# Kernel optimization log

Hardware: AMD Instinct MI355X
Metric: run time of the kernel (lower is better)

Reference implementation:

```python
import jax, jax.numpy as jnp
import numpy as np

N = 100000      # nodes (cells)
E = 1600000     # edges (kNN graph, avg degree 16)
DIM_IN = 128    # input features per cell
H = 8           # heads
C1 = 8          # per-head channels, layer 1 (concat -> 64)
DIM_OUT = 10    # classes (concat=False -> mean over heads)
NEG_SLOPE = 0.2


def setup_inputs() -> dict:
    key = jax.random.key(0)
    ks = jax.random.split(key, 10)
    s = 0.1
    return {
        "x": jax.random.normal(ks[0], (N, DIM_IN), dtype=jnp.float32),
        "edge_index": jax.random.randint(ks[1], (2, E), 0, N, dtype=jnp.int64),
        "W1": jax.random.normal(ks[2], (DIM_IN, H * C1), dtype=jnp.float32) * s,
        "a_src1": jax.random.normal(ks[3], (H, C1), dtype=jnp.float32) * s,
        "a_dst1": jax.random.normal(ks[4], (H, C1), dtype=jnp.float32) * s,
        "b1": jnp.zeros((H * C1,), dtype=jnp.float32),
        "W2": jax.random.normal(ks[5], (H * C1, H * DIM_OUT), dtype=jnp.float32) * s,
        "a_src2": jax.random.normal(ks[6], (H, DIM_OUT), dtype=jnp.float32) * s,
        "a_dst2": jax.random.normal(ks[7], (H, DIM_OUT), dtype=jnp.float32) * s,
        "b2": jnp.zeros((DIM_OUT,), dtype=jnp.float32),
    }


def _gat_layer(x, src, dst, W, a_src, a_dst, bias, concat, n):
    """PyG-style GATConv: gather -> edge attention -> segment softmax -> scatter."""
    h_, c_ = a_src.shape
    h = (x @ W).reshape(n, h_, c_)                       # [N, H, C]
    alpha_s = jnp.einsum('nhc,hc->nh', h, a_src)         # [N, H]
    alpha_d = jnp.einsum('nhc,hc->nh', h, a_dst)         # [N, H]
    # per-edge logits; PyG: message from src j to dst i, softmax over dst
    e = jax.nn.leaky_relu(alpha_s[src] + alpha_d[dst], NEG_SLOPE)  # [E, H]
    e_max = jax.ops.segment_max(e, dst, num_segments=n)            # [N, H]
    e = jnp.exp(e - e_max[dst])
    denom = jax.ops.segment_sum(e, dst, num_segments=n)            # [N, H]
    alpha = e / denom[dst]                                          # [E, H]
    msg = h[src] * alpha[:, :, None]                                # [E, H, C]
    out = jax.ops.segment_sum(msg, dst, num_segments=n)             # [N, H, C]
    out = out.reshape(n, h_ * c_) if concat else out.mean(axis=1)
    return out + bias


def reference(x, edge_index, W1, a_src1, a_dst1, b1, W2, a_src2, a_dst2, b2):
    n = x.shape[0]
    loops = jnp.arange(n, dtype=edge_index.dtype)
    src = jnp.concatenate([edge_index[0], loops])  # PyG adds self-loops by default
    dst = jnp.concatenate([edge_index[1], loops])
    h = _gat_layer(x, src, dst, W1, a_src1, a_dst1, b1, True, n)   # [N, 64]
    h = jax.nn.elu(h)
    h = _gat_layer(h, src, dst, W2, a_src2, a_dst2, b2, False, n)  # [N, dim_out]
    return jax.nn.log_softmax(h, axis=1)
```

## Files before the change

### kernel.cpp

```cpp
#include <hip/hip_runtime.h>
#include <hip/hip_bf16.h>
#include <cstdint>

#define CAP 64
#define SLICES 8
#define CHUNK_EDGES 8192

__device__ __forceinline__ float lrelu(float v) { return fmaxf(v, 0.2f * v); }

typedef float f32x2 __attribute__((ext_vector_type(2)));
__device__ __forceinline__ float2 q2f(unsigned short u) {
    f32x2 v = __builtin_amdgcn_cvt_pk_f32_fp8((int)u, false);
    return make_float2(v.x, v.y);
}
__device__ __forceinline__ int f2q4(float a, float b, float c, float d) {
    int p = __builtin_amdgcn_cvt_pk_fp8_f32(a, b, 0, false);
    p = __builtin_amdgcn_cvt_pk_fp8_f32(c, d, p, true);
    return p;
}
__device__ __forceinline__ float b2f(unsigned short u) { return __uint_as_float(((unsigned)u) << 16); }
__device__ __forceinline__ unsigned short f2b(float f) {
    unsigned u = __float_as_uint(f);
    return (unsigned short)((u + 0x7FFFu + ((u >> 16) & 1u)) >> 16);
}

__global__ __launch_bounds__(256, 8) void k_bg(const int* __restrict__ ei, int E, int N,
                                               int* __restrict__ cnt, int* __restrict__ bucket,
                                               const float* __restrict__ x,
                                               const float* __restrict__ W,
                                               const float* __restrict__ asrc,
                                               const float* __restrict__ adst,
                                               unsigned char* __restrict__ h1q,
                                               float* __restrict__ als, float* __restrict__ ald,
                                               int buildBlocks) {
    __shared__ float xs[32 * 132];
    if ((int)blockIdx.x < buildBlocks) {
        const int s = blockIdx.x & (SLICES - 1);
        const int chunk = blockIdx.x >> 3;
        const int sliceN = (N + SLICES - 1) / SLICES;
        const int lo = s * sliceN;
        const int hi = min(N, lo + sliceN);
        const int base = chunk * CHUNK_EDGES;
        const int end = min(base + CHUNK_EDGES, E);
        for (int e0 = base + (int)threadIdx.x * 4; e0 < end; e0 += 1024) {
            if (e0 + 4 <= end) {
                int4 d = *(const int4*)(ei + E + e0);
                int4 sv = *(const int4*)(ei + e0);
                if (d.x >= lo && d.x < hi) { int a = atomicAdd(&cnt[d.x], 1); if (a < CAP) bucket[(size_t)d.x * CAP + a] = sv.x; }
                if (d.y >= lo && d.y < hi) { int a = atomicAdd(&cnt[d.y], 1); if (a < CAP) bucket[(size_t)d.y * CAP + a] = sv.y; }
                if (d.z >= lo && d.z < hi) { int a = atomicAdd(&cnt[d.z], 1); if (a < CAP) bucket[(size_t)d.z * CAP + a] = sv.z; }
                if (d.w >= lo && d.w < hi) { int a = atomicAdd(&cnt[d.w], 1); if (a < CAP) bucket[(size_t)d.w * CAP + a] = sv.w; }
            } else {
                for (int e = e0; e < end; ++e) {
                    int d = ei[E + e];
                    if (d >= lo && d < hi) {
                        int a = atomicAdd(&cnt[d], 1);
                        if (a < CAP) bucket[(size_t)d * CAP + a] = ei[e];
                    }
                }
            }
        }
        return;
    }
    const int t = threadIdx.x;
    const int rowBase = ((int)blockIdx.x - buildBlocks) * 32;
#pragma unroll
    for (int i = 0; i < 4; ++i) {
        int g = i * 256 + t;
        int r = g >> 5, c4 = (g & 31) << 2;
        float4 v = make_float4(0.f, 0.f, 0.f, 0.f);
        int row = rowBase + r;
        if (row < N) v = *(const float4*)(x + (size_t)row * 128 + c4);
        *(float4*)(&xs[r * 132 + c4]) = v;
    }
    __syncthreads();
    const int tx = t & 15;
    const int ty = t >> 4;
    float acc[2][4] = {};
#pragma unroll 2
    for (int kc = 0; kc < 32; ++kc) {
        float4 a[2];
#pragma unroll
        for (int i = 0; i < 2; ++i) a[i] = *(const float4*)(&xs[(2 * ty + i) * 132 + kc * 4]);
        float4 w[4];
#pragma unroll
        for (int kk = 0; kk < 4; ++kk) w[kk] = *(const float4*)(W + (size_t)(kc * 4 + kk) * 64 + tx * 4);
#pragma unroll
        for (int i = 0; i < 2; ++i) {
            const float* ai = (const float*)&a[i];
#pragma unroll
            for (int j = 0; j < 4; ++j) {
                acc[i][j] += ai[0] * ((const float*)&w[0])[j]
                           + ai[1] * ((const float*)&w[1])[j]
                           + ai[2] * ((const float*)&w[2])[j]
                           + ai[3] * ((const float*)&w[3])[j];
            }
        }
    }
    const int h = tx >> 1;
    float4 av = *(const float4*)(asrc + tx * 4);
    float4 dv = *(const float4*)(adst + tx * 4);
#pragma unroll
    for (int i = 0; i < 2; ++i) {
        int row = rowBase + 2 * ty + i;
        float ps = acc[i][0] * av.x + acc[i][1] * av.y + acc[i][2] * av.z + acc[i][3] * av.w;
        float pd = acc[i][0] * dv.x + acc[i][1] * dv.y + acc[i][2] * dv.z + acc[i][3] * dv.w;
        ps += __shfl_xor(ps, 1);
        pd += __shfl_xor(pd, 1);
        if (row < N) {
            *(int*)(h1q + (size_t)row * 64 + tx * 4) = f2q4(acc[i][0], acc[i][1], acc[i][2], acc[i][3]);
            if ((tx & 1) == 0) {
                als[(size_t)row * 8 + h] = ps;
                ald[(size_t)row * 8 + h] = pd;
            }
        }
    }
}

__global__ __launch_bounds__(256) void k_gemm2(const float* __restrict__ hin,
                                               const float* __restrict__ W,
                                               const float* __restrict__ asrc,
                                               const float* __restrict__ adst,
                                               unsigned char* __restrict__ h2q,
                                               float* __restrict__ ald, int N) {
    __shared__ float xs[64 * 68];
    __shared__ float wt[80 * 68];
    const int t = threadIdx.x;
    const int rowBase = blockIdx.x * 64;
#pragma unroll
    for (int i = 0; i < 4; ++i) {
        int g = i * 256 + t;
        int r = g >> 4, c4 = (g & 15) << 2;
        float4 v = make_float4(0.f, 0.f, 0.f, 0.f);
        int row = rowBase + r;
        if (row < N) v = *(const float4*)(hin + (size_t)row * 64 + c4);
        *(float4*)(&xs[r * 68 + c4]) = v;
    }
#pragma unroll
    for (int i = 0; i < 20; ++i) {
        int g = i * 256 + t;
        int k = g / 80, c = g % 80;
        wt[c * 68 + k] = W[g];
    }
    __syncthreads();
    const int tx = t & 15;
    const int ty = t >> 4;
    float acc[4][5] = {};
#pragma unroll 4
    for (int kc = 0; kc < 16; ++kc) {
        float4 a[4];
#pragma unroll
        for (int i = 0; i < 4; ++i) a[i] = *(const float4*)(&xs[(4 * ty + i) * 68 + kc * 4]);
        float4 w[5];
#pragma unroll
        for (int j = 0; j < 5; ++j) w[j] = *(const float4*)(&wt[(5 * tx + j) * 68 + kc * 4]);
#pragma unroll
        for (int i = 0; i < 4; ++i) {
#pragma unroll
            for (int j = 0; j < 5; ++j) {
                acc[i][j] += a[i].x * w[j].x + a[i].y * w[j].y + a[i].z * w[j].z + a[i].w * w[j].w;
            }
        }
    }
    const int h = tx >> 1;
    float a2[5], d2[5];
#pragma unroll
    for (int j = 0; j < 5; ++j) { a2[j] = asrc[tx * 5 + j]; d2[j] = adst[tx * 5 + j]; }
    __syncthreads();
    unsigned char* qs = (unsigned char*)xs;
#pragma unroll
    for (int i = 0; i < 4; ++i) {
        int row = rowBase + 4 * ty + i;
        float ps = 0.f, pd = 0.f;
#pragma unroll
        for (int j = 0; j < 5; ++j) { ps += acc[i][j] * a2[j]; pd += acc[i][j] * d2[j]; }
        ps += __shfl_xor(ps, 1);
        pd += __shfl_xor(pd, 1);
        int p0 = __builtin_amdgcn_cvt_pk_fp8_f32(acc[i][0], acc[i][1], 0, false);
        int p1 = __builtin_amdgcn_cvt_pk_fp8_f32(acc[i][2], acc[i][3], 0, false);
        int p2 = __builtin_amdgcn_cvt_pk_fp8_f32(acc[i][4], acc[i][4], 0, false);
        unsigned char* q = qs + (4 * ty + i) * 96 + h * 12 + (tx & 1) * 5;
        q[0] = (unsigned char)(p0 & 0xFF);
        q[1] = (unsigned char)((p0 >> 8) & 0xFF);
        q[2] = (unsigned char)(p1 & 0xFF);
        q[3] = (unsigned char)((p1 >> 8) & 0xFF);
        q[4] = (unsigned char)(p2 & 0xFF);
        if ((tx & 1) == 0) {
            *(unsigned short*)(qs + (size_t)(4 * ty + i) * 96 + h * 12 + 10) = f2b(ps);
            if (row < N) ald[(size_t)row * 8 + h] = pd;
        }
    }
    __syncthreads();
    for (int g = t; g < 1536; g += 256) {
        int row = g / 24;
        if (rowBase + row < N)
            *(unsigned int*)(h2q + (size_t)rowBase * 96 + (size_t)g * 4) = ((unsigned int*)qs)[g];
    }
}

__global__ __launch_bounds__(256) void k_agg1(const int* __restrict__ cnt, const int* __restrict__ bucket,
                                              const unsigned char* __restrict__ h1q,
                                              const float* __restrict__ als, const float* __restrict__ ald,
                                              const float* __restrict__ b1,
                                              float* __restrict__ helu, int N) {
    int w = threadIdx.x >> 6, lane = threadIdx.x & 63;
    int e = lane >> 3, h = lane & 7;
    int n = blockIdx.x * 4 + w;
    bool act = n < N;
    float acc[8] = {};
    float den = 0.f;
    if (act) {
        float aldh = ald[(size_t)n * 8 + h];
        auto proc = [&](int s) {
            const unsigned char* row = h1q + (size_t)s * 64 + h * 8;
            int m0 = *(const int*)(row);
            int m1 = *(const int*)(row + 4);
            float a_s = als[(size_t)s * 8 + h];
            float wl = __expf(lrelu(a_s + aldh));
            den += wl;
            f32x2 v;
            v = __builtin_amdgcn_cvt_pk_f32_fp8(m0, false); acc[0] += wl * v.x; acc[1] += wl * v.y;
            v = __builtin_amdgcn_cvt_pk_f32_fp8(m0, true);  acc[2] += wl * v.x; acc[3] += wl * v.y;
            v = __builtin_amdgcn_cvt_pk_f32_fp8(m1, false); acc[4] += wl * v.x; acc[5] += wl * v.y;
            v = __builtin_amdgcn_cvt_pk_f32_fp8(m1, true);  acc[6] += wl * v.x; acc[7] += wl * v.y;
        };
        if (e == 0) proc(n);
        int k = min(cnt[n], CAP);
        const int* bp = bucket + (size_t)n * CAP;
        int i = e;
        int s = (i < k) ? bp[i] : -1;
        while (i < k) {
            int inext = i + 8;
            int snext = (inext < k) ? bp[inext] : -1;
            proc(s);
            i = inext; s = snext;
        }
    }
#pragma unroll
    for (int off = 8; off < 64; off <<= 1) {
        den += __shfl_xor(den, off);
#pragma unroll
        for (int j = 0; j < 8; ++j) acc[j] += __shfl_xor(acc[j], off);
    }
    if (act && e == 0) {
        float inv = 1.f / den;
        float o[8];
#pragma unroll
        for (int j = 0; j < 8; ++j) {
            float v = acc[j] * inv + b1[h * 8 + j];
            o[j] = v > 0.f ? v : __expf(v) - 1.f;
        }
        *(float4*)(helu + (size_t)n * 64 + h * 8)     = make_float4(o[0], o[1], o[2], o[3]);
        *(float4*)(helu + (size_t)n * 64 + h * 8 + 4) = make_float4(o[4], o[5], o[6], o[7]);
    }
}

__global__ __launch_bounds__(256) void k_agg2(const int* __restrict__ cnt, const int* __restrict__ bucket,
                                              const unsigned char* __restrict__ h2q,
                                              const float* __restrict__ ald,
                                              const float* __restrict__ b2,
                                              float* __restrict__ out, int N) {
    __shared__ float sm[4][80];
    int w = threadIdx.x >> 6, lane = threadIdx.x & 63;
    int e = lane >> 3, h = lane & 7;
    int n = blockIdx.x * 4 + w;
    bool act = n < N;
    float acc[10] = {};
    float den = 0.f;
    if (act) {
        float aldh = ald[(size_t)n * 8 + h];
        auto proc = [&](const unsigned char* row) {
            int m0 = *(const int*)(row);
            int m1 = *(const int*)(row + 4);
            int m2 = *(const int*)(row + 8);
            float a_s = b2f((unsigned short)(((unsigned)m2) >> 16));
            float wl = __expf(lrelu(a_s + aldh));
            den += wl;
            f32x2 v;
            v = __builtin_amdgcn_cvt_pk_f32_fp8(m0, false); acc[0] += wl * v.x; acc[1] += wl * v.y;
            v = __builtin_amdgcn_cvt_pk_f32_fp8(m0, true);  acc[2] += wl * v.x; acc[3] += wl * v.y;
            v = __builtin_amdgcn_cvt_pk_f32_fp8(m1, false); acc[4] += wl * v.x; acc[5] += wl * v.y;
            v = __builtin_amdgcn_cvt_pk_f32_fp8(m1, true);  acc[6] += wl * v.x; acc[7] += wl * v.y;
            v = __builtin_amdgcn_cvt_pk_f32_fp8(m2, false); acc[8] += wl * v.x; acc[9] += wl * v.y;
        };
        if (e == 0) proc(h2q + (size_t)n * 96 + h * 12);
        int k = min(cnt[n], CAP);
        const int* bp = bucket + (size_t)n * CAP;
        int i = e;
        int s = (i < k) ? bp[i] : -1;
        while (i < k) {
            int inext = i + 8;
            int snext = (inext < k) ? bp[inext] : -1;
            proc(h2q + (size_t)s * 96 + h * 12);
            i = inext; s = snext;
        }
    }
#pragma unroll
    for (int off = 8; off < 64; off <<= 1) {
        den += __shfl_xor(den, off);
#pragma unroll
        for (int j = 0; j < 10; ++j) acc[j] += __shfl_xor(acc[j], off);
    }
    if (act && e == 0) {
        float inv = 1.f / den;
#pragma unroll
        for (int j = 0; j < 10; ++j) sm[w][h * 10 + j] = acc[j] * inv;
    }
    __syncthreads();
    float m = 0.f;
    if (act && lane < 10) {
#pragma unroll
        for (int hh = 0; hh < 8; ++hh) m += sm[w][hh * 10 + lane];
        m = m * 0.125f + b2[lane];
    }
    __syncthreads();
    if (act && lane < 10) sm[w][lane] = m;
    __syncthreads();
    if (act && lane < 10) {
        float mx = -1e30f;
#pragma unroll
        for (int c = 0; c < 10; ++c) mx = fmaxf(mx, sm[w][c]);
        float ssum = 0.f;
#pragma unroll
        for (int c = 0; c < 10; ++c) ssum += __expf(sm[w][c] - mx);
        out[(size_t)n * 10 + lane] = m - mx - __logf(ssum);
    }
}

extern "C" void kernel_launch(void* const* d_in, const int* in_sizes, int n_in,
                              void* d_out, int out_size, void* d_ws, size_t ws_size,
                              hipStream_t stream) {
    const float* x     = (const float*)d_in[0];
    const int*   ei    = (const int*)d_in[1];
    const float* W1    = (const float*)d_in[2];
    const float* asrc1 = (const float*)d_in[3];
    const float* adst1 = (const float*)d_in[4];
    const float* b1    = (const float*)d_in[5];
    const float* W2    = (const float*)d_in[6];
    const float* asrc2 = (const float*)d_in[7];
    const float* adst2 = (const float*)d_in[8];
    const float* b2    = (const float*)d_in[9];
    float* out = (float*)d_out;

    int N = in_sizes[0] / 128;
    int E = in_sizes[1] / 2;

    char* base = (char*)d_ws;
    size_t off = 0;
    auto alloc = [&](size_t bytes) {
        char* p = base + off;
        off = (off + bytes + 255) & ~(size_t)255;
        return p;
    };
    int*            cnt    = (int*)alloc((size_t)N * 4);
    int*            bucket = (int*)alloc((size_t)N * CAP * 4);
    float*          helu   = (float*)alloc((size_t)N * 64 * 4);
    unsigned char*  hq     = (unsigned char*)alloc((size_t)N * 96);
    float*          als    = (float*)alloc((size_t)N * 8 * 4);
    float*          ald    = (float*)alloc((size_t)N * 8 * 4);
    (void)ws_size; (void)n_in; (void)out_size;

    (void)hipMemsetAsync(cnt, 0, (size_t)N * 4, stream);
    int chunks = (E + CHUNK_EDGES - 1) / CHUNK_EDGES;
    int buildBlocks = chunks * SLICES;
    int gemmBlocks = (N + 31) / 32;
    k_bg<<<buildBlocks + gemmBlocks, 256, 0, stream>>>(ei, E, N, cnt, bucket,
                                                       x, W1, asrc1, adst1, hq, als, ald, buildBlocks);
    k_agg1<<<(N + 3) / 4, 256, 0, stream>>>(cnt, bucket, hq, als, ald, b1, helu, N);
    k_gemm2<<<(N + 63) / 64, 256, 0, stream>>>(helu, W2, asrc2, adst2, hq, ald, N);
    k_agg2<<<(N + 3) / 4, 256, 0, stream>>>(cnt, bucket, hq, ald, b2, out, N);
}
```

Before: 356.9 us.

## Split fused build/GEMM kernel, shrink edge chunks, store source logits as bf16

Splits the combined bucket-build and layer-1 GEMM kernel into two separate launches. The build kernel now uses smaller edge chunks, giving more blocks and more parallelism for the atomic bucket fill. Source attention logits are stored as bf16 rather than fp32, halving that gather traffic in the layer-1 aggregation. The costs are an extra launch, the lost overlap between build and GEMM, and slightly reduced precision on the attention logits.

```diff
diff --git a/kernel.cpp b/kernel.cpp
--- a/kernel.cpp
+++ b/kernel.cpp
@@ -4,15 +4,11 @@
 
 #define CAP 64
 #define SLICES 8
-#define CHUNK_EDGES 8192
+#define CHUNK_EDGES 2048
 
 __device__ __forceinline__ float lrelu(float v) { return fmaxf(v, 0.2f * v); }
 
 typedef float f32x2 __attribute__((ext_vector_type(2)));
-__device__ __forceinline__ float2 q2f(unsigned short u) {
-    f32x2 v = __builtin_amdgcn_cvt_pk_f32_fp8((int)u, false);
-    return make_float2(v.x, v.y);
-}
 __device__ __forceinline__ int f2q4(float a, float b, float c, float d) {
     int p = __builtin_amdgcn_cvt_pk_fp8_f32(a, b, 0, false);
     p = __builtin_amdgcn_cvt_pk_fp8_f32(c, d, p, true);
@@ -24,46 +20,45 @@
     return (unsigned short)((u + 0x7FFFu + ((u >> 16) & 1u)) >> 16);
 }
 
-__global__ __launch_bounds__(256, 8) void k_bg(const int* __restrict__ ei, int E, int N,
-                                               int* __restrict__ cnt, int* __restrict__ bucket,
-                                               const float* __restrict__ x,
-                                               const float* __restrict__ W,
-                                               const float* __restrict__ asrc,
-                                               const float* __restrict__ adst,
-                                               unsigned char* __restrict__ h1q,
-                                               float* __restrict__ als, float* __restrict__ ald,
-                                               int buildBlocks) {
-    __shared__ float xs[32 * 132];
-    if ((int)blockIdx.x < buildBlocks) {
-        const int s = blockIdx.x & (SLICES - 1);
-        const int chunk = blockIdx.x >> 3;
-        const int sliceN = (N + SLICES - 1) / SLICES;
-        const int lo = s * sliceN;
-        const int hi = min(N, lo + sliceN);
-        const int base = chunk * CHUNK_EDGES;
-        const int end = min(base + CHUNK_EDGES, E);
-        for (int e0 = base + (int)threadIdx.x * 4; e0 < end; e0 += 1024) {
-            if (e0 + 4 <= end) {
-                int4 d = *(const int4*)(ei + E + e0);
-                int4 sv = *(const int4*)(ei + e0);
-                if (d.x >= lo && d.x < hi) { int a = atomicAdd(&cnt[d.x], 1); if (a < CAP) bucket[(size_t)d.x * CAP + a] = sv.x; }
-                if (d.y >= lo && d.y < hi) { int a = atomicAdd(&cnt[d.y], 1); if (a < CAP) bucket[(size_t)d.y * CAP + a] = sv.y; }
-                if (d.z >= lo && d.z < hi) { int a = atomicAdd(&cnt[d.z], 1); if (a < CAP) bucket[(size_t)d.z * CAP + a] = sv.z; }
-                if (d.w >= lo && d.w < hi) { int a = atomicAdd(&cnt[d.w], 1); if (a < CAP) bucket[(size_t)d.w * CAP + a] = sv.w; }
-            } else {
-                for (int e = e0; e < end; ++e) {
-                    int d = ei[E + e];
-                    if (d >= lo && d < hi) {
-                        int a = atomicAdd(&cnt[d], 1);
-                        if (a < CAP) bucket[(size_t)d * CAP + a] = ei[e];
-                    }
+__global__ __launch_bounds__(256) void k_build(const int* __restrict__ ei, int E, int N,
+                                               int* __restrict__ cnt, int* __restrict__ bucket) {
+    const int s = blockIdx.x & (SLICES - 1);
+    const int chunk = blockIdx.x >> 3;
+    const int sliceN = (N + SLICES - 1) / SLICES;
+    const int lo = s * sliceN;
+    const int hi = min(N, lo + sliceN);
+    const int base = chunk * CHUNK_EDGES;
+    const int end = min(base + CHUNK_EDGES, E);
+    for (int e0 = base + (int)threadIdx.x * 4; e0 < end; e0 += 1024) {
+        if (e0 + 4 <= end) {
+            int4 d = *(const int4*)(ei + E + e0);
+            int4 sv = *(const int4*)(ei + e0);
+            if (d.x >= lo && d.x < hi) { int a = atomicAdd(&cnt[d.x], 1); if (a < CAP) bucket[(size_t)d.x * CAP + a] = sv.x; }
+            if (d.y >= lo && d.y < hi) { int a = atomicAdd(&cnt[d.y], 1); if (a < CAP) bucket[(size_t)d.y * CAP + a] = sv.y; }
+            if (d.z >= lo && d.z < hi) { int a = atomicAdd(&cnt[d.z], 1); if (a < CAP) bucket[(size_t)d.z * CAP + a] = sv.z; }
+            if (d.w >= lo && d.w < hi) { int a = atomicAdd(&cnt[d.w], 1); if (a < CAP) bucket[(size_t)d.w * CAP + a] = sv.w; }
+        } else {
+            for (int e = e0; e < end; ++e) {
+                int d = ei[E + e];
+                if (d >= lo && d < hi) {
+                    int a = atomicAdd(&cnt[d], 1);
+                    if (a < CAP) bucket[(size_t)d * CAP + a] = ei[e];
                 }
             }
         }
-        return;
-    }
+    }
+}
+
+__global__ __launch_bounds__(256, 8) void k_gemm1(const float* __restrict__ x,
+                                                  const float* __restrict__ W,
+                                                  const float* __restrict__ asrc,
+                                                  const float* __restrict__ adst,
+                                                  unsigned char* __restrict__ h1q,
+                                                  unsigned short* __restrict__ alsb,
+                                                  float* __restrict__ ald, int N) {
+    __shared__ float xs[32 * 132];
     const int t = threadIdx.x;
-    const int rowBase = ((int)blockIdx.x - buildBlocks) * 32;
+    const int rowBase = blockIdx.x * 32;
 #pragma unroll
     for (int i = 0; i < 4; ++i) {
         int g = i * 256 + t;
@@ -110,7 +105,7 @@
         if (row < N) {
             *(int*)(h1q + (size_t)row * 64 + tx * 4) = f2q4(acc[i][0], acc[i][1], acc[i][2], acc[i][3]);
             if ((tx & 1) == 0) {
-                als[(size_t)row * 8 + h] = ps;
+                alsb[(size_t)row * 8 + h] = f2b(ps);
                 ald[(size_t)row * 8 + h] = pd;
             }
         }
@@ -200,7 +195,8 @@
 
 __global__ __launch_bounds__(256) void k_agg1(const int* __restrict__ cnt, const int* __restrict__ bucket,
                                               const unsigned char* __restrict__ h1q,
-                                              const float* __restrict__ als, const float* __restrict__ ald,
+                                              const unsigned short* __restrict__ alsb,
+                                              const float* __restrict__ ald,
                                               const float* __restrict__ b1,
                                               float* __restrict__ helu, int N) {
     int w = threadIdx.x >> 6, lane = threadIdx.x & 63;
@@ -215,7 +211,7 @@
             const unsigned char* row = h1q + (size_t)s * 64 + h * 8;
             int m0 = *(const int*)(row);
             int m1 = *(const int*)(row + 4);
-            float a_s = als[(size_t)s * 8 + h];
+            float a_s = b2f(alsb[(size_t)s * 8 + h]);
             float wl = __expf(lrelu(a_s + aldh));
             den += wl;
             f32x2 v;
@@ -356,17 +352,15 @@
     int*            bucket = (int*)alloc((size_t)N * CAP * 4);
     float*          helu   = (float*)alloc((size_t)N * 64 * 4);
     unsigned char*  hq     = (unsigned char*)alloc((size_t)N * 96);
-    float*          als    = (float*)alloc((size_t)N * 8 * 4);
+    unsigned short* alsb   = (unsigned short*)alloc((size_t)N * 8 * 2);
     float*          ald    = (float*)alloc((size_t)N * 8 * 4);
     (void)ws_size; (void)n_in; (void)out_size;
 
     (void)hipMemsetAsync(cnt, 0, (size_t)N * 4, stream);
     int chunks = (E + CHUNK_EDGES - 1) / CHUNK_EDGES;
-    int buildBlocks = chunks * SLICES;
-    int gemmBlocks = (N + 31) / 32;
-    k_bg<<<buildBlocks + gemmBlocks, 256, 0, stream>>>(ei, E, N, cnt, bucket,
-                                                       x, W1, asrc1, adst1, hq, als, ald, buildBlocks);
-    k_agg1<<<(N + 3) / 4, 256, 0, stream>>>(cnt, bucket, hq, als, ald, b1, helu, N);
+    k_build<<<chunks * SLICES, 256, 0, stream>>>(ei, E, N, cnt, bucket);
+    k_gemm1<<<(N + 31) / 32, 256, 0, stream>>>(x, W1, asrc1, adst1, hq, alsb, ald, N);
+    k_agg1<<<(N + 3) / 4, 256, 0, stream>>>(cnt, bucket, hq, alsb, ald, b1, helu, N);
     k_gemm2<<<(N + 63) / 64, 256, 0, stream>>>(helu, W2, asrc2, adst2, hq, ald, N);
     k_agg2<<<(N + 3) / 4, 256, 0, stream>>>(cnt, bucket, hq, ald, b2, out, N);
 }
```

Result: slower. 371.8 us (+4.2%).
